# Kernel tuning notes

Hardware: AMD Instinct MI355X
Metric: run time of the kernel (lower is better)

## Reference

```python
import jax, jax.numpy as jnp
import numpy as np

KERNEL_SIZE = 5
KERNEL_NUM = 64
STRIDE = 1
PRIOR_VAR = 1.0


def setup_inputs() -> dict:
    key = jax.random.key(0)
    k1, k2 = jax.random.split(key)
    mu_in = jax.random.normal(k1, (128, 128, 128, 3), dtype=jnp.float32)
    # init: normal stddev 0.05 for w_mu, constant -4.6 for w_sigma
    w_mu = 0.05 * jax.random.normal(k2, (KERNEL_SIZE, KERNEL_SIZE, 3, KERNEL_NUM), dtype=jnp.float32)
    w_sigma = jnp.full((KERNEL_NUM,), -4.6, dtype=jnp.float32)
    return {"mu_in": mu_in, "w_mu": w_mu, "w_sigma": w_sigma}


def kl_regularizer_conv(mu, logvar):
    k = mu.shape[-1]
    mu2 = mu.reshape(-1, k)              # [k*k*C, kernel_num]
    n = mu2.shape[0]
    kl = -jnp.mean(1.0 + logvar
                   - jnp.log1p(jnp.exp(logvar)) / PRIOR_VAR
                   - jnp.sum(jnp.square(mu2), axis=0) / (n * PRIOR_VAR))
    kl = jnp.where(jnp.isnan(kl), jnp.float32(1e-05), kl)
    kl = jnp.where(jnp.isinf(kl), jnp.float32(1e-05), kl)
    return kl


def reference(mu_in, w_mu, w_sigma):
    B, H, W, C = mu_in.shape
    ks = KERNEL_SIZE
    kl_conv = kl_regularizer_conv(w_mu, w_sigma)
    w_sigma_2 = jnp.log1p(jnp.exp(w_sigma))  # softplus

    dn = ('NHWC', 'HWIO', 'NHWC')
    mu_out = jax.lax.conv_general_dilated(
        mu_in, w_mu, window_strides=(STRIDE, STRIDE), padding='VALID',
        dimension_numbers=dn)  # [B, Ho, Wo, kernel_num]

    # Per-patch sum of squares == sum-pool conv over squared input summed over C
    # (mathematically identical to extract_patches -> square -> sum, no im2col blowup)
    sq = jnp.sum(jnp.square(mu_in), axis=-1, keepdims=True)  # [B,H,W,1]
    ones_k = jnp.ones((ks, ks, 1, 1), dtype=mu_in.dtype)
    patch_ss = jax.lax.conv_general_dilated(
        sq, ones_k, window_strides=(STRIDE, STRIDE), padding='VALID',
        dimension_numbers=dn)  # [B, Ho, Wo, 1]
    x_dim = jnp.float32(ks * ks * C)
    # broadcast: softplus(w_sigma)[kn] * (sum_sq / x_dim)[B,Ho,Wo,1]
    Sigma_out = w_sigma_2 * (patch_ss / x_dim)  # [B, Ho, Wo, kernel_num]

    Ho = mu_out.shape[1]
    Sigma_out = Sigma_out.reshape(B, Ho, Ho, KERNEL_NUM)
    return (mu_out, Sigma_out, kl_conv)
```

## Files before the change

### kernel.cpp

```cpp
#include <hip/hip_runtime.h>
#include <hip/hip_bf16.h>
#include <math.h>

#define KN 64
#define HO 124
#define KP 104
#define NOUT (128LL * 124 * 124 * 64)
#define NG 31

#define WS_SSN_OFF 0ULL
#define WS_WBF_OFF 7872512ULL
#define WS_SP_OFF 7885824ULL

typedef short bfrag8 __attribute__((ext_vector_type(8)));
typedef float ffrag4 __attribute__((ext_vector_type(4)));

__device__ __forceinline__ unsigned short f2bf(float f) {
    union { float f; unsigned u; } x;
    x.f = f;
    unsigned r = x.u + 0x7fffu + ((x.u >> 16) & 1u);
    return (unsigned short)(r >> 16);
}
__device__ __forceinline__ unsigned pack2(float a, float b) {
    return (unsigned)f2bf(a) | ((unsigned)f2bf(b) << 16);
}

__device__ __forceinline__ int im_off(int row, int wo, int half) {
    return (((row * 128 + wo) * 32) + half * 16) ^ (((wo >> 2) & 7) << 4);
}

__global__ void prep_kernel(const float* __restrict__ w_mu,
                            const float* __restrict__ w_sigma,
                            unsigned short* __restrict__ w_bf,
                            float* __restrict__ sp_out) {
    const int tid = threadIdx.x;
    const int n = tid >> 2;
    const int kbase = (tid & 3) * 26;
#pragma unroll
    for (int kk = 0; kk < 26; ++kk) {
        const int k = kbase + kk;
        float v = 0.f;
        if (k < 80) {
            const int r = k >> 4, t = k & 15;
            if (t < 15) v = w_mu[(r * 15 + t) * KN + n];
        }
        w_bf[n * KP + k] = f2bf(v);
    }
    if (tid < KN) sp_out[tid] = log1pf(expf(w_sigma[tid]));
}

__global__ void kl_kernel(const float* __restrict__ w_mu,
                          const float* __restrict__ w_sigma,
                          float* __restrict__ out_kl) {
    int kn = threadIdx.x;
    float s = 0.f;
#pragma unroll
    for (int i = 0; i < 75; ++i) {
        float m = w_mu[i * KN + kn];
        s = fmaf(m, m, s);
    }
    float lv = w_sigma[kn];
    float sp = log1pf(expf(lv));
    float val = 1.0f + lv - sp - s * (1.0f / 75.0f);
#pragma unroll
    for (int off = 32; off > 0; off >>= 1) val += __shfl_down(val, off);
    if (kn == 0) {
        float kl = -(val / 64.0f);
        if (isnan(kl) || isinf(kl)) kl = 1e-5f;
        out_kl[0] = kl;
    }
}

__global__ void ssn_kernel(const float* __restrict__ mu_in,
                           float* __restrict__ ssn_ws) {
    __shared__ __align__(16) float s_cs[8 * 128];
    const int bid = blockIdx.x;
    const int b = bid / NG;
    const int ho0 = (bid % NG) * 4;
    const int tid = threadIdx.x;

    {
        const int r = tid >> 5;
        const int c4 = (tid & 31) << 2;
        const float* p = mu_in + ((size_t)(b * 128 + ho0 + r) * 384 + c4 * 3);
        float4 f0 = reinterpret_cast<const float4*>(p)[0];
        float4 f1 = reinterpret_cast<const float4*>(p)[1];
        float4 f2 = reinterpret_cast<const float4*>(p)[2];
        float4 cs;
        cs.x = f0.x * f0.x + f0.y * f0.y + f0.z * f0.z;
        cs.y = f0.w * f0.w + f1.x * f1.x + f1.y * f1.y;
        cs.z = f1.z * f1.z + f1.w * f1.w + f2.x * f2.x;
        cs.w = f2.y * f2.y + f2.z * f2.z + f2.w * f2.w;
        *reinterpret_cast<float4*>(&s_cs[r * 128 + c4]) = cs;
    }
    __syncthreads();

#pragma unroll
    for (int it = 0; it < 2; ++it) {
        const int idx = tid + it * 256;
        const int hl = idx >> 7, wo = idx & 127;
        if (wo < HO) {
            float s = 0.f;
#pragma unroll
            for (int r = 0; r < 5; ++r) {
                const float* cr = &s_cs[(hl + r) * 128 + wo];
                s += cr[0] + cr[1] + cr[2] + cr[3] + cr[4];
            }
            ssn_ws[((size_t)(b * HO) + ho0 + hl) * HO + wo] = s * (1.0f / 75.0f);
        }
    }
}

__global__ __launch_bounds__(256) void sigma_kernel(
    const float* __restrict__ ssn_ws, const float* __restrict__ sp_in,
    float4* __restrict__ sig_out) {
    const long long TOT = 128LL * 124 * 124 * 16;
    const long long NT = (long long)gridDim.x * 256;
    const long long g0 = (long long)blockIdx.x * 256 + threadIdx.x;
    const float4 sp4 = reinterpret_cast<const float4*>(sp_in)[g0 & 15];

    long long g = g0;
    for (; g + 3 * NT < TOT; g += 4 * NT) {
        const float s0 = ssn_ws[g >> 4];
        const float s1 = ssn_ws[(g + NT) >> 4];
        const float s2 = ssn_ws[(g + 2 * NT) >> 4];
        const float s3 = ssn_ws[(g + 3 * NT) >> 4];
        sig_out[g] = make_float4(sp4.x * s0, sp4.y * s0, sp4.z * s0, sp4.w * s0);
        sig_out[g + NT] =
            make_float4(sp4.x * s1, sp4.y * s1, sp4.z * s1, sp4.w * s1);
        sig_out[g + 2 * NT] =
            make_float4(sp4.x * s2, sp4.y * s2, sp4.z * s2, sp4.w * s2);
        sig_out[g + 3 * NT] =
            make_float4(sp4.x * s3, sp4.y * s3, sp4.z * s3, sp4.w * s3);
    }
    for (; g < TOT; g += NT) {
        const float s = ssn_ws[g >> 4];
        sig_out[g] = make_float4(sp4.x * s, sp4.y * s, sp4.z * s, sp4.w * s);
    }
}

template <int OFF>
__device__ __forceinline__ void im_fill(const float* __restrict__ mu_in,
                                        unsigned short* s_im, int b, int ho0,
                                        int lane, int wo) {
#pragma unroll
    for (int j = 0; j < 4; ++j) {
        const int row = ((lane >> 5) << 2) + j;
        uint4* dst0 =
            reinterpret_cast<uint4*>((char*)s_im + im_off(row, wo, 0));
        uint4* dst1 =
            reinterpret_cast<uint4*>((char*)s_im + im_off(row, wo, 1));
        if (wo >= 124) {
            *dst0 = make_uint4(0u, 0u, 0u, 0u);
            *dst1 = make_uint4(0u, 0u, 0u, 0u);
            continue;
        }
        const float* p =
            mu_in + ((size_t)(b * 128 + ho0 + row) * 384 + wo * 3 - OFF);
        float w[20];
        float4 f;
        f = reinterpret_cast<const float4*>(p)[0];
        w[0] = f.x; w[1] = f.y; w[2] = f.z; w[3] = f.w;
        f = reinterpret_cast<const float4*>(p)[1];
        w[4] = f.x; w[5] = f.y; w[6] = f.z; w[7] = f.w;
        f = reinterpret_cast<const float4*>(p)[2];
        w[8] = f.x; w[9] = f.y; w[10] = f.z; w[11] = f.w;
        f = reinterpret_cast<const float4*>(p)[3];
        w[12] = f.x; w[13] = f.y; w[14] = f.z; w[15] = f.w;
        if (OFF >= 2) {
            f = reinterpret_cast<const float4*>(p)[4];
            w[16] = f.x; w[17] = f.y; w[18] = f.z; w[19] = f.w;
        } else {
            w[16] = 0.f; w[17] = 0.f; w[18] = 0.f; w[19] = 0.f;
        }
        unsigned u0 = pack2(w[OFF + 0], w[OFF + 1]);
        unsigned u1 = pack2(w[OFF + 2], w[OFF + 3]);
        unsigned u2 = pack2(w[OFF + 4], w[OFF + 5]);
        unsigned u3 = pack2(w[OFF + 6], w[OFF + 7]);
        unsigned u4 = pack2(w[OFF + 8], w[OFF + 9]);
        unsigned u5 = pack2(w[OFF + 10], w[OFF + 11]);
        unsigned u6 = pack2(w[OFF + 12], w[OFF + 13]);
        unsigned u7 = pack2(w[OFF + 14], 0.0f);
        *dst0 = make_uint4(u0, u1, u2, u3);
        *dst1 = make_uint4(u4, u5, u6, u7);
    }
}

__global__ __launch_bounds__(256, 4) void conv_mu_kernel(
    const float* __restrict__ mu_in,
    const unsigned short* __restrict__ w_bf,
    float* __restrict__ mu_out) {

    __shared__ __align__(16) unsigned short s_im[8 * 128 * 16];

    const int bid = blockIdx.x;
    const int b = bid / NG;
    const int ho0 = (bid % NG) * 4;
    const int tid = threadIdx.x;
    const int lane = tid & 63;
    const int wid = tid >> 6;
    const int llo = lane & 15;
    const int lhi = lane >> 4;

    bfrag8 afr[4][3];
#pragma unroll
    for (int mt = 0; mt < 4; ++mt)
#pragma unroll
        for (int ks = 0; ks < 3; ++ks)
            afr[mt][ks] = *reinterpret_cast<const bfrag8*>(
                &w_bf[(mt * 16 + llo) * KP + ks * 32 + lhi * 8]);

    {
        const int wo = wid + ((lane & 31) << 2);
        switch (wid) {
            case 0: im_fill<0>(mu_in, s_im, b, ho0, lane, wo); break;
            case 1: im_fill<3>(mu_in, s_im, b, ho0, lane, wo); break;
            case 2: im_fill<2>(mu_in, s_im, b, ho0, lane, wo); break;
            default: im_fill<1>(mu_in, s_im, b, ho0, lane, wo); break;
        }
    }
    __syncthreads();

#pragma unroll
    for (int hl = 0; hl < 4; ++hl) {
        ffrag4 acc[2][4];
#pragma unroll
        for (int nt = 0; nt < 2; ++nt)
#pragma unroll
            for (int mt = 0; mt < 4; ++mt)
                acc[nt][mt] = (ffrag4){0.f, 0.f, 0.f, 0.f};

#pragma unroll
        for (int nt = 0; nt < 2; ++nt) {
            const int wo = (wid * 2 + nt) * 16 + llo;
#pragma unroll
            for (int ks = 0; ks < 3; ++ks) {
                const int k0 = ks * 32 + lhi * 8;
                const int r = k0 >> 4;
                bfrag8 bfr = (bfrag8){0, 0, 0, 0, 0, 0, 0, 0};
                if (r < 5) {
                    bfr = *reinterpret_cast<const bfrag8*>(
                        (char*)s_im + im_off(hl + r, wo, (k0 & 15) >> 3));
                }
#pragma unroll
                for (int mt = 0; mt < 4; ++mt)
                    acc[nt][mt] = __builtin_amdgcn_mfma_f32_16x16x32_bf16(
                        afr[mt][ks], bfr, acc[nt][mt], 0, 0, 0);
            }
        }

        const size_t orow = (size_t)(b * HO + ho0 + hl) * (size_t)(HO * KN);
#pragma unroll
        for (int nt = 0; nt < 2; ++nt) {
            const int wo = (wid * 2 + nt) * 16 + llo;
            if (wo < HO) {
                const size_t obase = orow + (size_t)wo * KN;
#pragma unroll
                for (int mt = 0; mt < 4; ++mt) {
                    const int knb = mt * 16 + lhi * 4;
                    *reinterpret_cast<float4*>(&mu_out[obase + knb]) =
                        make_float4(acc[nt][mt][0], acc[nt][mt][1],
                                    acc[nt][mt][2], acc[nt][mt][3]);
                }
            }
        }
    }
}

extern "C" void kernel_launch(void* const* d_in, const int* in_sizes, int n_in,
                              void* d_out, int out_size, void* d_ws,
                              size_t ws_size, hipStream_t stream) {
    const float* mu_in = (const float*)d_in[0];
    const float* w_mu = (const float*)d_in[1];
    const float* w_sigma = (const float*)d_in[2];
    float* out = (float*)d_out;

    float* mu_out = out;
    float* sig_out = out + NOUT;
    float* kl_out = out + 2 * NOUT;

    char* ws = (char*)d_ws;
    float* ssn_ws = (float*)(ws + WS_SSN_OFF);
    unsigned short* w_bf = (unsigned short*)(ws + WS_WBF_OFF);
    float* sp_ws = (float*)(ws + WS_SP_OFF);

    prep_kernel<<<1, 256, 0, stream>>>(w_mu, w_sigma, w_bf, sp_ws);
    ssn_kernel<<<128 * NG, 256, 0, stream>>>(mu_in, ssn_ws);
    conv_mu_kernel<<<128 * NG, 256, 0, stream>>>(mu_in, w_bf, mu_out);
    sigma_kernel<<<2048, 256, 0, stream>>>(ssn_ws, sp_ws,
                                           (float4*)sig_out);
    kl_kernel<<<1, 64, 0, stream>>>(w_mu, w_sigma, kl_out);
}
```

Before: 228.5 us.

## Interleave sigma broadcast blocks into conv kernel grid and fold KL into prep

The conv and sigma-broadcast kernels are merged into one launch where every third block writes Sigma_out and the other two run the MFMA conv, so memory-bound writes overlap with compute-heavy blocks. The KL reduction moves into the prep kernel, which removes a launch. This trades two separate kernels for a heterogeneous grid whose sigma blocks each do a fixed 62-iteration strided loop. That loop assumes exactly 1984 sigma blocks cover the output evenly.

Measured after the change: 269.5 us. +17.9%, slower.

```diff
diff --git a/kernel.cpp b/kernel.cpp
--- a/kernel.cpp
+++ b/kernel.cpp
@@ -7,6 +7,8 @@
 #define KP 104
 #define NOUT (128LL * 124 * 124 * 64)
 #define NG 31
+#define NCONV (128 * NG)
+#define NSIG 1984
 
 #define WS_SSN_OFF 0ULL
 #define WS_WBF_OFF 7872512ULL
@@ -32,7 +34,8 @@
 __global__ void prep_kernel(const float* __restrict__ w_mu,
                             const float* __restrict__ w_sigma,
                             unsigned short* __restrict__ w_bf,
-                            float* __restrict__ sp_out) {
+                            float* __restrict__ sp_out,
+                            float* __restrict__ out_kl) {
     const int tid = threadIdx.x;
     const int n = tid >> 2;
     const int kbase = (tid & 3) * 26;
@@ -47,27 +50,24 @@
         w_bf[n * KP + k] = f2bf(v);
     }
     if (tid < KN) sp_out[tid] = log1pf(expf(w_sigma[tid]));
-}
-
-__global__ void kl_kernel(const float* __restrict__ w_mu,
-                          const float* __restrict__ w_sigma,
-                          float* __restrict__ out_kl) {
-    int kn = threadIdx.x;
-    float s = 0.f;
-#pragma unroll
-    for (int i = 0; i < 75; ++i) {
-        float m = w_mu[i * KN + kn];
-        s = fmaf(m, m, s);
-    }
-    float lv = w_sigma[kn];
-    float sp = log1pf(expf(lv));
-    float val = 1.0f + lv - sp - s * (1.0f / 75.0f);
-#pragma unroll
-    for (int off = 32; off > 0; off >>= 1) val += __shfl_down(val, off);
-    if (kn == 0) {
-        float kl = -(val / 64.0f);
-        if (isnan(kl) || isinf(kl)) kl = 1e-5f;
-        out_kl[0] = kl;
+
+    if (tid < 64) {
+        float s = 0.f;
+#pragma unroll
+        for (int i = 0; i < 75; ++i) {
+            float m = w_mu[i * KN + tid];
+            s = fmaf(m, m, s);
+        }
+        float lv = w_sigma[tid];
+        float sp = log1pf(expf(lv));
+        float val = 1.0f + lv - sp - s * (1.0f / 75.0f);
+#pragma unroll
+        for (int off = 32; off > 0; off >>= 1) val += __shfl_down(val, off);
+        if (tid == 0) {
+            float kl = -(val / 64.0f);
+            if (isnan(kl) || isinf(kl)) kl = 1e-5f;
+            out_kl[0] = kl;
+        }
     }
 }
 
@@ -108,34 +108,6 @@
             }
             ssn_ws[((size_t)(b * HO) + ho0 + hl) * HO + wo] = s * (1.0f / 75.0f);
         }
-    }
-}
-
-__global__ __launch_bounds__(256) void sigma_kernel(
-    const float* __restrict__ ssn_ws, const float* __restrict__ sp_in,
-    float4* __restrict__ sig_out) {
-    const long long TOT = 128LL * 124 * 124 * 16;
-    const long long NT = (long long)gridDim.x * 256;
-    const long long g0 = (long long)blockIdx.x * 256 + threadIdx.x;
-    const float4 sp4 = reinterpret_cast<const float4*>(sp_in)[g0 & 15];
-
-    long long g = g0;
-    for (; g + 3 * NT < TOT; g += 4 * NT) {
-        const float s0 = ssn_ws[g >> 4];
-        const float s1 = ssn_ws[(g + NT) >> 4];
-        const float s2 = ssn_ws[(g + 2 * NT) >> 4];
-        const float s3 = ssn_ws[(g + 3 * NT) >> 4];
-        sig_out[g] = make_float4(sp4.x * s0, sp4.y * s0, sp4.z * s0, sp4.w * s0);
-        sig_out[g + NT] =
-            make_float4(sp4.x * s1, sp4.y * s1, sp4.z * s1, sp4.w * s1);
-        sig_out[g + 2 * NT] =
-            make_float4(sp4.x * s2, sp4.y * s2, sp4.z * s2, sp4.w * s2);
-        sig_out[g + 3 * NT] =
-            make_float4(sp4.x * s3, sp4.y * s3, sp4.z * s3, sp4.w * s3);
-    }
-    for (; g < TOT; g += NT) {
-        const float s = ssn_ws[g >> 4];
-        sig_out[g] = make_float4(sp4.x * s, sp4.y * s, sp4.z * s, sp4.w * s);
     }
 }
 
@@ -186,17 +158,33 @@
     }
 }
 
-__global__ __launch_bounds__(256, 4) void conv_mu_kernel(
+__global__ __launch_bounds__(256, 4) void fused_kernel(
     const float* __restrict__ mu_in,
     const unsigned short* __restrict__ w_bf,
-    float* __restrict__ mu_out) {
+    const float* __restrict__ ssn_ws, const float* __restrict__ sp_in,
+    float* __restrict__ mu_out, float4* __restrict__ sig_out) {
 
     __shared__ __align__(16) unsigned short s_im[8 * 128 * 16];
 
     const int bid = blockIdx.x;
-    const int b = bid / NG;
-    const int ho0 = (bid % NG) * 4;
     const int tid = threadIdx.x;
+
+    if (bid % 3 == 2) {
+        const long long NT = (long long)NSIG * 256;
+        long long g = (long long)(bid / 3) * 256 + tid;
+        const float4 sp4 = reinterpret_cast<const float4*>(sp_in)[tid & 15];
+#pragma unroll 2
+        for (int it = 0; it < 62; ++it, g += NT) {
+            const float s = ssn_ws[g >> 4];
+            sig_out[g] =
+                make_float4(sp4.x * s, sp4.y * s, sp4.z * s, sp4.w * s);
+        }
+        return;
+    }
+
+    const int cid = (bid / 3) * 2 + (bid % 3);
+    const int b = cid / NG;
+    const int ho0 = (cid % NG) * 4;
     const int lane = tid & 63;
     const int wid = tid >> 6;
     const int llo = lane & 15;
@@ -284,10 +272,8 @@
     unsigned short* w_bf = (unsigned short*)(ws + WS_WBF_OFF);
     float* sp_ws = (float*)(ws + WS_SP_OFF);
 
-    prep_kernel<<<1, 256, 0, stream>>>(w_mu, w_sigma, w_bf, sp_ws);
+    prep_kernel<<<1, 256, 0, stream>>>(w_mu, w_sigma, w_bf, sp_ws, kl_out);
     ssn_kernel<<<128 * NG, 256, 0, stream>>>(mu_in, ssn_ws);
-    conv_mu_kernel<<<128 * NG, 256, 0, stream>>>(mu_in, w_bf, mu_out);
-    sigma_kernel<<<2048, 256, 0, stream>>>(ssn_ws, sp_ws,
-                                           (float4*)sig_out);
-    kl_kernel<<<1, 64, 0, stream>>>(w_mu, w_sigma, kl_out);
-}
+    fused_kernel<<<NCONV / 2 * 3, 256, 0, stream>>>(
+        mu_in, w_bf, ssn_ws, sp_ws, mu_out, (float4*)sig_out);
+}
```

## Make conv kernel persistent over four groups with prefetch of next input tile

Applied to the files above, without the earlier changes.

The conv kernel now launches a quarter as many blocks, and each block processes four row groups in turn. During the MFMA compute for the current group it loads and packs the next group's input rows into registers, then writes them to LDS between barriers, so global load latency overlaps with compute. The KL computation moves into the prep kernel to drop one launch, and launch bounds are relaxed from 4 to 3 waves per SIMD. The trade-offs are higher register pressure, lower occupancy, fewer blocks for load balancing, and extra barriers.

New measurement: 263.3 us. 1.15x slower.

```diff
diff --git a/kernel.cpp b/kernel.cpp
--- a/kernel.cpp
+++ b/kernel.cpp
@@ -7,6 +7,9 @@
 #define KP 104
 #define NOUT (128LL * 124 * 124 * 64)
 #define NG 31
+#define NCONV (128 * NG)
+#define GPB 4
+#define NBLK (NCONV / GPB)
 
 #define WS_SSN_OFF 0ULL
 #define WS_WBF_OFF 7872512ULL
@@ -29,10 +32,20 @@
     return (((row * 128 + wo) * 32) + half * 16) ^ (((wo >> 2) & 7) << 4);
 }
 
+__device__ __forceinline__ void block_sync_nodrain() {
+    __builtin_amdgcn_sched_barrier(0);
+    __builtin_amdgcn_s_barrier();
+    __builtin_amdgcn_sched_barrier(0);
+}
+__device__ __forceinline__ void lds_flush() {
+    asm volatile("s_waitcnt lgkmcnt(0)" ::: "memory");
+}
+
 __global__ void prep_kernel(const float* __restrict__ w_mu,
                             const float* __restrict__ w_sigma,
                             unsigned short* __restrict__ w_bf,
-                            float* __restrict__ sp_out) {
+                            float* __restrict__ sp_out,
+                            float* __restrict__ out_kl) {
     const int tid = threadIdx.x;
     const int n = tid >> 2;
     const int kbase = (tid & 3) * 26;
@@ -47,27 +60,24 @@
         w_bf[n * KP + k] = f2bf(v);
     }
     if (tid < KN) sp_out[tid] = log1pf(expf(w_sigma[tid]));
-}
-
-__global__ void kl_kernel(const float* __restrict__ w_mu,
-                          const float* __restrict__ w_sigma,
-                          float* __restrict__ out_kl) {
-    int kn = threadIdx.x;
-    float s = 0.f;
-#pragma unroll
-    for (int i = 0; i < 75; ++i) {
-        float m = w_mu[i * KN + kn];
-        s = fmaf(m, m, s);
-    }
-    float lv = w_sigma[kn];
-    float sp = log1pf(expf(lv));
-    float val = 1.0f + lv - sp - s * (1.0f / 75.0f);
-#pragma unroll
-    for (int off = 32; off > 0; off >>= 1) val += __shfl_down(val, off);
-    if (kn == 0) {
-        float kl = -(val / 64.0f);
-        if (isnan(kl) || isinf(kl)) kl = 1e-5f;
-        out_kl[0] = kl;
+
+    if (tid < 64) {
+        float s = 0.f;
+#pragma unroll
+        for (int i = 0; i < 75; ++i) {
+            float m = w_mu[i * KN + tid];
+            s = fmaf(m, m, s);
+        }
+        float lv = w_sigma[tid];
+        float sp = log1pf(expf(lv));
+        float val = 1.0f + lv - sp - s * (1.0f / 75.0f);
+#pragma unroll
+        for (int off = 32; off > 0; off >>= 1) val += __shfl_down(val, off);
+        if (tid == 0) {
+            float kl = -(val / 64.0f);
+            if (isnan(kl) || isinf(kl)) kl = 1e-5f;
+            out_kl[0] = kl;
+        }
     }
 }
 
@@ -140,67 +150,70 @@
 }
 
 template <int OFF>
-__device__ __forceinline__ void im_fill(const float* __restrict__ mu_in,
-                                        unsigned short* s_im, int b, int ho0,
-                                        int lane, int wo) {
-#pragma unroll
-    for (int j = 0; j < 4; ++j) {
-        const int row = ((lane >> 5) << 2) + j;
-        uint4* dst0 =
-            reinterpret_cast<uint4*>((char*)s_im + im_off(row, wo, 0));
-        uint4* dst1 =
-            reinterpret_cast<uint4*>((char*)s_im + im_off(row, wo, 1));
-        if (wo >= 124) {
-            *dst0 = make_uint4(0u, 0u, 0u, 0u);
-            *dst1 = make_uint4(0u, 0u, 0u, 0u);
-            continue;
-        }
-        const float* p =
-            mu_in + ((size_t)(b * 128 + ho0 + row) * 384 + wo * 3 - OFF);
-        float w[20];
-        float4 f;
-        f = reinterpret_cast<const float4*>(p)[0];
-        w[0] = f.x; w[1] = f.y; w[2] = f.z; w[3] = f.w;
-        f = reinterpret_cast<const float4*>(p)[1];
-        w[4] = f.x; w[5] = f.y; w[6] = f.z; w[7] = f.w;
-        f = reinterpret_cast<const float4*>(p)[2];
-        w[8] = f.x; w[9] = f.y; w[10] = f.z; w[11] = f.w;
-        f = reinterpret_cast<const float4*>(p)[3];
-        w[12] = f.x; w[13] = f.y; w[14] = f.z; w[15] = f.w;
-        if (OFF >= 2) {
-            f = reinterpret_cast<const float4*>(p)[4];
-            w[16] = f.x; w[17] = f.y; w[18] = f.z; w[19] = f.w;
-        } else {
-            w[16] = 0.f; w[17] = 0.f; w[18] = 0.f; w[19] = 0.f;
-        }
-        unsigned u0 = pack2(w[OFF + 0], w[OFF + 1]);
-        unsigned u1 = pack2(w[OFF + 2], w[OFF + 3]);
-        unsigned u2 = pack2(w[OFF + 4], w[OFF + 5]);
-        unsigned u3 = pack2(w[OFF + 6], w[OFF + 7]);
-        unsigned u4 = pack2(w[OFF + 8], w[OFF + 9]);
-        unsigned u5 = pack2(w[OFF + 10], w[OFF + 11]);
-        unsigned u6 = pack2(w[OFF + 12], w[OFF + 13]);
-        unsigned u7 = pack2(w[OFF + 14], 0.0f);
-        *dst0 = make_uint4(u0, u1, u2, u3);
-        *dst1 = make_uint4(u4, u5, u6, u7);
-    }
-}
-
-__global__ __launch_bounds__(256, 4) void conv_mu_kernel(
+__device__ __forceinline__ void pair_load(const float* __restrict__ mu_in,
+                                          int b, int ho0, int row, int wo,
+                                          float4 f[5]) {
+    if (wo >= 124) return;
+    const float4* p = reinterpret_cast<const float4*>(
+        mu_in + ((size_t)(b * 128 + ho0 + row) * 384 + wo * 3 - OFF));
+    f[0] = p[0];
+    f[1] = p[1];
+    f[2] = p[2];
+    f[3] = p[3];
+    if constexpr (OFF >= 2) f[4] = p[4];
+}
+
+template <int OFF>
+__device__ __forceinline__ void pair_pack(const float4 f[5], int wo, uint4& lo,
+                                          uint4& hi) {
+    if (wo >= 124) {
+        lo = make_uint4(0u, 0u, 0u, 0u);
+        hi = make_uint4(0u, 0u, 0u, 0u);
+        return;
+    }
+    float w[20];
+#pragma unroll
+    for (int q = 0; q < 4; ++q) {
+        w[4 * q] = f[q].x;
+        w[4 * q + 1] = f[q].y;
+        w[4 * q + 2] = f[q].z;
+        w[4 * q + 3] = f[q].w;
+    }
+    if constexpr (OFF >= 2) {
+        w[16] = f[4].x;
+        w[17] = f[4].y;
+        w[18] = f[4].z;
+        w[19] = f[4].w;
+    }
+    lo = make_uint4(pack2(w[OFF + 0], w[OFF + 1]), pack2(w[OFF + 2], w[OFF + 3]),
+                    pack2(w[OFF + 4], w[OFF + 5]), pack2(w[OFF + 6], w[OFF + 7]));
+    hi = make_uint4(pack2(w[OFF + 8], w[OFF + 9]),
+                    pack2(w[OFF + 10], w[OFF + 11]),
+                    pack2(w[OFF + 12], w[OFF + 13]), pack2(w[OFF + 14], 0.0f));
+}
+
+#define WID_DISPATCH(...)                                   \
+    switch (wid) {                                          \
+        case 0: { constexpr int OFF = 0; __VA_ARGS__; } break; \
+        case 1: { constexpr int OFF = 3; __VA_ARGS__; } break; \
+        case 2: { constexpr int OFF = 2; __VA_ARGS__; } break; \
+        default: { constexpr int OFF = 1; __VA_ARGS__; } break; \
+    }
+
+__global__ __launch_bounds__(256, 3) void conv_mu_kernel(
     const float* __restrict__ mu_in,
     const unsigned short* __restrict__ w_bf,
     float* __restrict__ mu_out) {
 
     __shared__ __align__(16) unsigned short s_im[8 * 128 * 16];
 
-    const int bid = blockIdx.x;
-    const int b = bid / NG;
-    const int ho0 = (bid % NG) * 4;
     const int tid = threadIdx.x;
     const int lane = tid & 63;
     const int wid = tid >> 6;
     const int llo = lane & 15;
     const int lhi = lane >> 4;
+    const int wo_my = wid + ((lane & 31) << 2);
+    const int rb = (lane >> 5) << 2;
 
     bfrag8 afr[4][3];
 #pragma unroll
@@ -210,60 +223,120 @@
             afr[mt][ks] = *reinterpret_cast<const bfrag8*>(
                 &w_bf[(mt * 16 + llo) * KP + ks * 32 + lhi * 8]);
 
+    float4 f[5];
+    uint4 pk[8];
+    int cid = blockIdx.x;
+
     {
-        const int wo = wid + ((lane & 31) << 2);
-        switch (wid) {
-            case 0: im_fill<0>(mu_in, s_im, b, ho0, lane, wo); break;
-            case 1: im_fill<3>(mu_in, s_im, b, ho0, lane, wo); break;
-            case 2: im_fill<2>(mu_in, s_im, b, ho0, lane, wo); break;
-            default: im_fill<1>(mu_in, s_im, b, ho0, lane, wo); break;
-        }
-    }
-    __syncthreads();
-
-#pragma unroll
-    for (int hl = 0; hl < 4; ++hl) {
-        ffrag4 acc[2][4];
-#pragma unroll
-        for (int nt = 0; nt < 2; ++nt)
-#pragma unroll
-            for (int mt = 0; mt < 4; ++mt)
-                acc[nt][mt] = (ffrag4){0.f, 0.f, 0.f, 0.f};
-
-#pragma unroll
-        for (int nt = 0; nt < 2; ++nt) {
-            const int wo = (wid * 2 + nt) * 16 + llo;
-#pragma unroll
-            for (int ks = 0; ks < 3; ++ks) {
-                const int k0 = ks * 32 + lhi * 8;
-                const int r = k0 >> 4;
-                bfrag8 bfr = (bfrag8){0, 0, 0, 0, 0, 0, 0, 0};
-                if (r < 5) {
-                    bfr = *reinterpret_cast<const bfrag8*>(
-                        (char*)s_im + im_off(hl + r, wo, (k0 & 15) >> 3));
+        const int b0 = cid / NG, h00 = (cid % NG) * 4;
+        WID_DISPATCH(pair_load<OFF>(mu_in, b0, h00, rb + 0, wo_my, f));
+        WID_DISPATCH(pair_pack<OFF>(f, wo_my, pk[0], pk[1]));
+        WID_DISPATCH(pair_load<OFF>(mu_in, b0, h00, rb + 1, wo_my, f));
+        WID_DISPATCH(pair_pack<OFF>(f, wo_my, pk[2], pk[3]));
+        WID_DISPATCH(pair_load<OFF>(mu_in, b0, h00, rb + 2, wo_my, f));
+        WID_DISPATCH(pair_pack<OFF>(f, wo_my, pk[4], pk[5]));
+        WID_DISPATCH(pair_load<OFF>(mu_in, b0, h00, rb + 3, wo_my, f));
+        WID_DISPATCH(pair_pack<OFF>(f, wo_my, pk[6], pk[7]));
+#pragma unroll
+        for (int j = 0; j < 4; ++j) {
+            *reinterpret_cast<uint4*>((char*)s_im + im_off(rb + j, wo_my, 0)) =
+                pk[2 * j];
+            *reinterpret_cast<uint4*>((char*)s_im + im_off(rb + j, wo_my, 1)) =
+                pk[2 * j + 1];
+        }
+        lds_flush();
+        block_sync_nodrain();
+    }
+
+#pragma unroll
+    for (int g = 0; g < GPB; ++g) {
+        const int b = cid / NG;
+        const int ho0 = (cid % NG) * 4;
+        const int ncid = cid + NBLK;
+        const bool hn = (g < GPB - 1);
+        const int nb = hn ? ncid / NG : 0;
+        const int nh0 = hn ? (ncid % NG) * 4 : 0;
+
+#pragma unroll
+        for (int hl = 0; hl < 4; ++hl) {
+            ffrag4 acc[2][4];
+#pragma unroll
+            for (int nt = 0; nt < 2; ++nt)
+#pragma unroll
+                for (int mt = 0; mt < 4; ++mt)
+                    acc[nt][mt] = (ffrag4){0.f, 0.f, 0.f, 0.f};
+
+#pragma unroll
+            for (int nt = 0; nt < 2; ++nt) {
+                const int wo = (wid * 2 + nt) * 16 + llo;
+#pragma unroll
+                for (int ks = 0; ks < 3; ++ks) {
+                    const int k0 = ks * 32 + lhi * 8;
+                    const int r = k0 >> 4;
+                    bfrag8 bfr = (bfrag8){0, 0, 0, 0, 0, 0, 0, 0};
+                    if (r < 5) {
+                        bfr = *reinterpret_cast<const bfrag8*>(
+                            (char*)s_im + im_off(hl + r, wo, (k0 & 15) >> 3));
+                    }
+#pragma unroll
+                    for (int mt = 0; mt < 4; ++mt)
+                        acc[nt][mt] = __builtin_amdgcn_mfma_f32_16x16x32_bf16(
+                            afr[mt][ks], bfr, acc[nt][mt], 0, 0, 0);
                 }
-#pragma unroll
-                for (int mt = 0; mt < 4; ++mt)
-                    acc[nt][mt] = __builtin_amdgcn_mfma_f32_16x16x32_bf16(
-                        afr[mt][ks], bfr, acc[nt][mt], 0, 0, 0);
-            }
-        }
-
-        const size_t orow = (size_t)(b * HO + ho0 + hl) * (size_t)(HO * KN);
-#pragma unroll
-        for (int nt = 0; nt < 2; ++nt) {
-            const int wo = (wid * 2 + nt) * 16 + llo;
-            if (wo < HO) {
-                const size_t obase = orow + (size_t)wo * KN;
-#pragma unroll
-                for (int mt = 0; mt < 4; ++mt) {
-                    const int knb = mt * 16 + lhi * 4;
-                    *reinterpret_cast<float4*>(&mu_out[obase + knb]) =
-                        make_float4(acc[nt][mt][0], acc[nt][mt][1],
-                                    acc[nt][mt][2], acc[nt][mt][3]);
+            }
+
+            const size_t orow =
+                (size_t)(b * HO + ho0 + hl) * (size_t)(HO * KN);
+#pragma unroll
+            for (int nt = 0; nt < 2; ++nt) {
+                const int wo = (wid * 2 + nt) * 16 + llo;
+                if (wo < HO) {
+                    const size_t obase = orow + (size_t)wo * KN;
+#pragma unroll
+                    for (int mt = 0; mt < 4; ++mt) {
+                        const int knb = mt * 16 + lhi * 4;
+                        *reinterpret_cast<float4*>(&mu_out[obase + knb]) =
+                            make_float4(acc[nt][mt][0], acc[nt][mt][1],
+                                        acc[nt][mt][2], acc[nt][mt][3]);
+                    }
                 }
             }
-        }
+
+            if (hn) {
+                if (hl == 0) {
+                    WID_DISPATCH(
+                        pair_load<OFF>(mu_in, nb, nh0, rb + 0, wo_my, f));
+                } else if (hl == 1) {
+                    WID_DISPATCH(pair_pack<OFF>(f, wo_my, pk[0], pk[1]));
+                    WID_DISPATCH(
+                        pair_load<OFF>(mu_in, nb, nh0, rb + 1, wo_my, f));
+                } else if (hl == 2) {
+                    WID_DISPATCH(pair_pack<OFF>(f, wo_my, pk[2], pk[3]));
+                    WID_DISPATCH(
+                        pair_load<OFF>(mu_in, nb, nh0, rb + 2, wo_my, f));
+                } else {
+                    WID_DISPATCH(pair_pack<OFF>(f, wo_my, pk[4], pk[5]));
+                    WID_DISPATCH(
+                        pair_load<OFF>(mu_in, nb, nh0, rb + 3, wo_my, f));
+                    WID_DISPATCH(pair_pack<OFF>(f, wo_my, pk[6], pk[7]));
+                }
+            }
+        }
+
+        if (hn) {
+            block_sync_nodrain();
+#pragma unroll
+            for (int j = 0; j < 4; ++j) {
+                *reinterpret_cast<uint4*>((char*)s_im +
+                                          im_off(rb + j, wo_my, 0)) = pk[2 * j];
+                *reinterpret_cast<uint4*>((char*)s_im +
+                                          im_off(rb + j, wo_my, 1)) =
+                    pk[2 * j + 1];
+            }
+            lds_flush();
+            block_sync_nodrain();
+        }
+        cid = ncid;
     }
 }
 
@@ -284,10 +357,8 @@
     unsigned short* w_bf = (unsigned short*)(ws + WS_WBF_OFF);
     float* sp_ws = (float*)(ws + WS_SP_OFF);
 
-    prep_kernel<<<1, 256, 0, stream>>>(w_mu, w_sigma, w_bf, sp_ws);
+    prep_kernel<<<1, 256, 0, stream>>>(w_mu, w_sigma, w_bf, sp_ws, kl_out);
     ssn_kernel<<<128 * NG, 256, 0, stream>>>(mu_in, ssn_ws);
-    conv_mu_kernel<<<128 * NG, 256, 0, stream>>>(mu_in, w_bf, mu_out);
-    sigma_kernel<<<2048, 256, 0, stream>>>(ssn_ws, sp_ws,
-                                           (float4*)sig_out);
-    kl_kernel<<<1, 64, 0, stream>>>(w_mu, w_sigma, kl_out);
-}
+    conv_mu_kernel<<<NBLK, 256, 0, stream>>>(mu_in, w_bf, mu_out);
+    sigma_kernel<<<2048, 256, 0, stream>>>(ssn_ws, sp_ws, (float4*)sig_out);
+}
```
